# Kernel optimization log

Measured on AMD Instinct MI355X. Metric: run time of the kernel, lower is better.

## Reference

```python
import jax, jax.numpy as jnp
import numpy as np

D = 1024
H = 8          # MHA fallback num_heads
DH = D // H
DFF = 4096     # mlp_ratio * hidden_size
EPS = 1e-6


def _ln(x, g, b):
    mu = jnp.mean(x, axis=-1, keepdims=True)
    var = jnp.mean((x - mu) ** 2, axis=-1, keepdims=True)
    return (x - mu) * jax.lax.rsqrt(var + EPS) * g + b


def setup_inputs() -> dict:
    key = jax.random.key(0)
    ks = jax.random.split(key, 16)
    s = 0.02
    return {
        "x": jax.random.normal(ks[0], (8, 1024, D), jnp.float32),
        "c": jax.random.normal(ks[1], (8, D), jnp.float32),
        # Mamba-block (attention fallback) params
        "m_ada_w": jax.random.normal(ks[2], (D, 3 * D), jnp.float32) * s,
        "m_ada_b": jnp.zeros((3 * D,), jnp.float32),
        "m_norm_g": jnp.ones((D,), jnp.float32),
        "m_norm_b": jnp.zeros((D,), jnp.float32),
        "in_proj_w": jax.random.normal(ks[3], (3 * D, D), jnp.float32) * s,
        "in_proj_b": jnp.zeros((3 * D,), jnp.float32),
        "out_proj_w": jax.random.normal(ks[4], (D, D), jnp.float32) * s,
        "out_proj_b": jnp.zeros((D,), jnp.float32),
        # FeedForward-block params
        "f_ada_w": jax.random.normal(ks[5], (D, 3 * D), jnp.float32) * s,
        "f_ada_b": jnp.zeros((3 * D,), jnp.float32),
        "f_norm_g": jnp.ones((D,), jnp.float32),
        "f_norm_b": jnp.zeros((D,), jnp.float32),
        "w1": jax.random.normal(ks[6], (D, DFF), jnp.float32) * s,
        "b1": jnp.zeros((DFF,), jnp.float32),
        "w2": jax.random.normal(ks[7], (DFF, D), jnp.float32) * s,
        "b2": jnp.zeros((D,), jnp.float32),
    }


def reference(x, c, m_ada_w, m_ada_b, m_norm_g, m_norm_b, in_proj_w, in_proj_b,
              out_proj_w, out_proj_b, f_ada_w, f_ada_b, f_norm_g, f_norm_b,
              w1, b1, w2, b2):
    B, N, _ = x.shape
    # ---- MambaBlock (MHA fallback), dropout = identity (eval) ----
    mod = jax.nn.silu(c) @ m_ada_w + m_ada_b              # (B, 3D)
    shift, scale, gate = jnp.split(mod, 3, axis=-1)
    h = _ln(x, m_norm_g, m_norm_b)
    h = h * (1.0 + scale[:, None, :]) + shift[:, None, :]
    qkv = h @ in_proj_w.T + in_proj_b                      # (B, N, 3D)
    q, k, v = jnp.split(qkv, 3, axis=-1)
    q = q.reshape(B, N, H, DH)
    k = k.reshape(B, N, H, DH)
    v = v.reshape(B, N, H, DH)
    scores = jnp.einsum("bqhd,bkhd->bhqk", q, k) / np.sqrt(DH).astype(np.float32)
    attn = jax.nn.softmax(scores, axis=-1)
    o = jnp.einsum("bhqk,bkhd->bqhd", attn, v).reshape(B, N, D)
    o = o @ out_proj_w.T + out_proj_b
    x = x + gate[:, None, :] * o
    # ---- FeedForward block ----
    mod2 = jax.nn.silu(c) @ f_ada_w + f_ada_b
    shift2, scale2, gate2 = jnp.split(mod2, 3, axis=-1)
    h = _ln(x, f_norm_g, f_norm_b)
    h = h * (1.0 + scale2[:, None, :]) + shift2[:, None, :]
    h = jax.nn.gelu(h @ w1 + b1, approximate=False) @ w2 + b2
    return x + gate2[:, None, :] * h
```

## Files before the change

### kernel.cpp

```cpp
#include <hip/hip_runtime.h>

typedef __bf16 bf16x8 __attribute__((ext_vector_type(8)));
typedef float f32x4 __attribute__((ext_vector_type(4)));

__device__ __forceinline__ unsigned short f2bf(float f) {
    unsigned int u = __float_as_uint(f);
    unsigned int r = (u + 0x7FFFu + ((u >> 16) & 1u)) >> 16;
    return (unsigned short)r;
}

__device__ __forceinline__ void gload16(const void* g, void* l) {
    __builtin_amdgcn_global_load_lds(
        (const __attribute__((address_space(1))) unsigned int*)g,
        (__attribute__((address_space(3))) unsigned int*)l, 16, 0, 0);
}

__device__ __forceinline__ void barrier_raw() {
    asm volatile("" ::: "memory");
    __builtin_amdgcn_s_barrier();
    asm volatile("" ::: "memory");
}

__device__ __forceinline__ void vmwait0() {
    asm volatile("s_waitcnt vmcnt(0)" ::: "memory");
}

__device__ __forceinline__ float gelu_fast(float u) {
    float z = 1.595769122f * u + 0.071354816f * u * u * u;
    return u / (1.f + __expf(-z));
}

__global__ __launch_bounds__(256) void f2b4(const float* __restrict__ in,
                                            unsigned short* __restrict__ out) {
    size_t i = ((size_t)blockIdx.x * 256 + threadIdx.x) * 4;
    float4 v = *(const float4*)(in + i);
    ushort4 o;
    o.x = f2bf(v.x); o.y = f2bf(v.y); o.z = f2bf(v.z); o.w = f2bf(v.w);
    *(ushort4*)(out + i) = o;
}

__global__ __launch_bounds__(256) void transpose_f2b(const float* __restrict__ in,
                                                     unsigned short* __restrict__ out,
                                                     int R, int C) {
    __shared__ float tile[32][33];
    int r0 = blockIdx.y * 32, c0 = blockIdx.x * 32;
    int tx = threadIdx.x & 31, ty = threadIdx.x >> 5;
#pragma unroll
    for (int i = 0; i < 4; i++) {
        int r = ty + i * 8;
        tile[r][tx] = in[(size_t)(r0 + r) * C + c0 + tx];
    }
    __syncthreads();
#pragma unroll
    for (int i = 0; i < 4; i++) {
        int r = ty + i * 8;
        out[(size_t)(c0 + r) * R + r0 + tx] = f2bf(tile[tx][r]);
    }
}

__global__ __launch_bounds__(256) void ada_mod_part(const float* __restrict__ c,
                                                    const float* __restrict__ W,
                                                    float* __restrict__ partial) {
    __shared__ float sc[8 * 64];
    int kc = blockIdx.y * 64;
    for (int i = threadIdx.x; i < 512; i += 256) {
        int b = i >> 6, k = i & 63;
        float cv = c[b * 1024 + kc + k];
        sc[i] = cv / (1.f + __expf(-cv));
    }
    __syncthreads();
    int j = blockIdx.x * 256 + threadIdx.x;
    float acc[8] = {0, 0, 0, 0, 0, 0, 0, 0};
    for (int k = 0; k < 64; k++) {
        float w = W[(size_t)(kc + k) * 3072 + j];
#pragma unroll
        for (int b = 0; b < 8; b++) acc[b] += sc[b * 64 + k] * w;
    }
#pragma unroll
    for (int b = 0; b < 8; b++) partial[((size_t)blockIdx.y * 8 + b) * 3072 + j] = acc[b];
}

__global__ __launch_bounds__(256) void ada_reduce(const float* __restrict__ partial,
                                                  const float* __restrict__ bias,
                                                  float* __restrict__ out) {
    int idx = blockIdx.x * 256 + threadIdx.x;
    int b = idx / 3072;
    int jj = idx - b * 3072;
    float s = bias[jj];
#pragma unroll
    for (int ch = 0; ch < 16; ch++) s += partial[((size_t)ch * 8 + b) * 3072 + jj];
    out[idx] = s;
}

__global__ __launch_bounds__(256) void ln_mod_kernel(const float* __restrict__ x,
                                                     const float* __restrict__ gamma,
                                                     const float* __restrict__ beta,
                                                     const float* __restrict__ mods,
                                                     unsigned short* __restrict__ out) {
    int row = blockIdx.x;
    int b = row >> 10;
    float4 v = ((const float4*)(x + (size_t)row * 1024))[threadIdx.x];
    float s = v.x + v.y + v.z + v.w;
    float s2 = v.x * v.x + v.y * v.y + v.z * v.z + v.w * v.w;
#pragma unroll
    for (int d = 1; d < 64; d <<= 1) { s += __shfl_xor(s, d); s2 += __shfl_xor(s2, d); }
    __shared__ float red[8];
    int lane = threadIdx.x & 63, wid = threadIdx.x >> 6;
    if (lane == 0) { red[wid] = s; red[4 + wid] = s2; }
    __syncthreads();
    float S = red[0] + red[1] + red[2] + red[3];
    float S2 = red[4] + red[5] + red[6] + red[7];
    float mu = S * (1.f / 1024.f);
    float var = S2 * (1.f / 1024.f) - mu * mu;
    float rs = rsqrtf(var + 1e-6f);
    const float* mrow = mods + b * 3072;
    int j0 = threadIdx.x * 4;
    float hv[4] = {v.x, v.y, v.z, v.w};
    ushort4 o;
    unsigned short* op = (unsigned short*)&o;
#pragma unroll
    for (int i = 0; i < 4; i++) {
        int j = j0 + i;
        float hh = (hv[i] - mu) * rs * gamma[j] + beta[j];
        hh = hh * (1.f + mrow[1024 + j]) + mrow[j];
        op[i] = f2bf(hh);
    }
    *(ushort4*)(out + (size_t)row * 1024 + j0) = o;
}

template <int EP>
__global__ __launch_bounds__(256, 2) void gemmw(const unsigned short* __restrict__ A,
                                                const unsigned short* __restrict__ Bt,
                                                int N, int K, int nx,
                                                const float* __restrict__ bias,
                                                unsigned short* __restrict__ outb,
                                                unsigned short* __restrict__ vt) {
    constexpr int AE = 128 * 32;
    constexpr int BE = 256 * 32;
    extern __shared__ __align__(16) char smem[];
    __bf16* As = (__bf16*)smem;
    __bf16* Bs = As + 3 * AE;

    int tid = threadIdx.x, lane = tid & 63, wid = tid >> 6;
    int t = lane & 15, g = lane >> 4;
    int xk2 = ((t >> 1) & 3) * 8;

    int nwg = gridDim.x, chunk = nwg >> 3;
    int swz = (blockIdx.x & 7) * chunk + (blockIdx.x >> 3);
    int bx = swz % nx, by = swz / nx;
    int rowA0 = by * 128, colB0 = bx * 256;

    int rin = tid >> 2, cblk = tid & 3;
    int scol = (cblk ^ ((rin >> 1) & 3)) * 8;

    auto stage = [&](int nb, int kt) {
        int k0 = kt << 5;
        gload16(A + (size_t)(rowA0 + rin) * K + k0 + scol, As + nb * AE + tid * 8);
        gload16(A + (size_t)(rowA0 + 64 + rin) * K + k0 + scol,
                As + nb * AE + 2048 + tid * 8);
#pragma unroll
        for (int sl = 0; sl < 4; sl++)
            gload16(Bt + (size_t)(colB0 + sl * 64 + rin) * K + k0 + scol,
                    Bs + nb * BE + sl * 2048 + tid * 8);
    };

    f32x4 acc[8][4];
#pragma unroll
    for (int m = 0; m < 8; m++)
#pragma unroll
        for (int n = 0; n < 4; n++) acc[m][n] = (f32x4){0.f, 0.f, 0.f, 0.f};

    int NT = K >> 5;
    stage(0, 0);
    if (NT > 1) {
        stage(1, 1);
        asm volatile("s_waitcnt vmcnt(6)" ::: "memory");
    } else {
        vmwait0();
    }
    barrier_raw();

    int cur = 0, tgt = 2;
#pragma unroll 1
    for (int kt = 0; kt < NT; ++kt) {
        bool deep = (kt + 2) < NT;
        bool more = (kt + 1) < NT;
        if (deep) stage(tgt, kt + 2);
        const __bf16* Ac = As + cur * AE;
        const __bf16* Bc = Bs + cur * BE;

        bf16x8 b[4];
#pragma unroll
        for (int n = 0; n < 4; n++)
            b[n] = *(const bf16x8*)&Bc[(wid * 64 + n * 16 + t) * 32 + ((g * 8) ^ xk2)];

        __builtin_amdgcn_s_setprio(1);
#pragma unroll
        for (int mh = 0; mh < 2; mh++) {
            bf16x8 a[4];
#pragma unroll
            for (int m4 = 0; m4 < 4; m4++)
                a[m4] = *(const bf16x8*)&Ac[(mh * 64 + m4 * 16 + t) * 32 + ((g * 8) ^ xk2)];
#pragma unroll
            for (int m4 = 0; m4 < 4; m4++)
#pragma unroll
                for (int n = 0; n < 4; n++)
                    acc[mh * 4 + m4][n] =
                        __builtin_amdgcn_mfma_f32_16x16x32_bf16(a[m4], b[n], acc[mh * 4 + m4][n], 0, 0, 0);
        }
        __builtin_amdgcn_s_setprio(0);

        if (more) {
            if (deep) {
                asm volatile("s_waitcnt vmcnt(6)" ::: "memory");
            } else {
                vmwait0();
            }
            barrier_raw();
        }
        cur = (cur == 2) ? 0 : cur + 1;
        tgt = (tgt == 2) ? 0 : tgt + 1;
    }

    int col0 = colB0 + wid * 64;
    bool vpart = (EP == 0) && (colB0 >= 2048);
#pragma unroll
    for (int m = 0; m < 8; m++)
#pragma unroll
        for (int n = 0; n < 4; n++) {
            int col = col0 + n * 16 + t;
            if (EP == 0 && vpart) {
                int hcol = col - 2048;
                int hh = hcol >> 7, d = hcol & 127;
                int bb = rowA0 >> 10;
                int ntok = (rowA0 + m * 16 + g * 4) & 1023;
                float bs = bias[col];
                ushort4 vv;
                vv.x = f2bf(acc[m][n][0] + bs);
                vv.y = f2bf(acc[m][n][1] + bs);
                vv.z = f2bf(acc[m][n][2] + bs);
                vv.w = f2bf(acc[m][n][3] + bs);
                *(ushort4*)(vt + (((size_t)(bb * 8 + hh) * 128 + d) * 1024 + ntok)) = vv;
            } else {
#pragma unroll
                for (int r = 0; r < 4; r++) {
                    int row = rowA0 + m * 16 + g * 4 + r;
                    float v = acc[m][n][r];
                    if (EP == 0) {
                        outb[(size_t)row * N + col] = f2bf(v + bias[col]);
                    } else {
                        outb[(size_t)row * N + col] = f2bf(gelu_fast(v + bias[col]));
                    }
                }
            }
        }
}

template <int EP>
__global__ __launch_bounds__(256, 4) void gemmo(const unsigned short* __restrict__ A,
                                                const unsigned short* __restrict__ Bt,
                                                int N, int K, int nx,
                                                const float* __restrict__ bias,
                                                const float* __restrict__ xres,
                                                const float* __restrict__ mods,
                                                float* __restrict__ outf) {
    constexpr int AE = 128 * 32;
    constexpr int BE = 128 * 32;
    extern __shared__ __align__(16) char smem[];
    __bf16* As = (__bf16*)smem;
    __bf16* Bs = As + 3 * AE;

    int tid = threadIdx.x, lane = tid & 63, wid = tid >> 6;
    int wr = wid >> 1, wc = wid & 1;
    int t = lane & 15, g = lane >> 4;
    int xk2 = ((t >> 1) & 3) * 8;

    int nwg = gridDim.x, chunk = nwg >> 3;
    int swz = (blockIdx.x & 7) * chunk + (blockIdx.x >> 3);
    int bx = swz % nx, by = swz / nx;
    int rowA0 = by * 128, colB0 = bx * 128;

    int rin = tid >> 2, cblk = tid & 3;
    int scol = (cblk ^ ((rin >> 1) & 3)) * 8;

    auto stage = [&](int nb, int kt) {
        int k0 = kt << 5;
        gload16(A + (size_t)(rowA0 + rin) * K + k0 + scol, As + nb * AE + tid * 8);
        gload16(A + (size_t)(rowA0 + 64 + rin) * K + k0 + scol,
                As + nb * AE + 2048 + tid * 8);
        gload16(Bt + (size_t)(colB0 + rin) * K + k0 + scol, Bs + nb * BE + tid * 8);
        gload16(Bt + (size_t)(colB0 + 64 + rin) * K + k0 + scol,
                Bs + nb * BE + 2048 + tid * 8);
    };

    f32x4 acc[4][4];
#pragma unroll
    for (int m = 0; m < 4; m++)
#pragma unroll
        for (int n = 0; n < 4; n++) acc[m][n] = (f32x4){0.f, 0.f, 0.f, 0.f};

    int NT = K >> 5;
    stage(0, 0);
    if (NT > 1) {
        stage(1, 1);
        asm volatile("s_waitcnt vmcnt(4)" ::: "memory");
    } else {
        vmwait0();
    }
    barrier_raw();

    int cur = 0, tgt = 2;
#pragma unroll 1
    for (int kt = 0; kt < NT; ++kt) {
        bool deep = (kt + 2) < NT;
        bool more = (kt + 1) < NT;
        if (deep) stage(tgt, kt + 2);
        const __bf16* Ac = As + cur * AE;
        const __bf16* Bc = Bs + cur * BE;

        bf16x8 a[4], b[4];
#pragma unroll
        for (int m = 0; m < 4; m++)
            a[m] = *(const bf16x8*)&Ac[(wr * 64 + m * 16 + t) * 32 + ((g * 8) ^ xk2)];
#pragma unroll
        for (int n = 0; n < 4; n++)
            b[n] = *(const bf16x8*)&Bc[(wc * 64 + n * 16 + t) * 32 + ((g * 8) ^ xk2)];

        __builtin_amdgcn_s_setprio(1);
#pragma unroll
        for (int m = 0; m < 4; m++)
#pragma unroll
            for (int n = 0; n < 4; n++)
                acc[m][n] = __builtin_amdgcn_mfma_f32_16x16x32_bf16(a[m], b[n], acc[m][n], 0, 0, 0);
        __builtin_amdgcn_s_setprio(0);

        if (more) {
            if (deep) {
                asm volatile("s_waitcnt vmcnt(4)" ::: "memory");
            } else {
                vmwait0();
            }
            barrier_raw();
        }
        cur = (cur == 2) ? 0 : cur + 1;
        tgt = (tgt == 2) ? 0 : tgt + 1;
    }

    int row0 = rowA0 + wr * 64, col0 = colB0 + wc * 64;
#pragma unroll
    for (int m = 0; m < 4; m++)
#pragma unroll
        for (int n = 0; n < 4; n++) {
            int col = col0 + n * 16 + t;
#pragma unroll
            for (int r = 0; r < 4; r++) {
                int row = row0 + m * 16 + g * 4 + r;
                float v = acc[m][n][r];
                int bb = row >> 10;
                float gt = mods[bb * 3072 + 2048 + col];
                if (EP == 1) {
                    outf[(size_t)row * 1024 + col] =
                        xres[(size_t)row * 1024 + col] + gt * (v + bias[col]);
                } else {
                    outf[(size_t)row * 1024 + col] += gt * (v + bias[col]);
                }
            }
        }
}

__global__ __launch_bounds__(512, 4) void attn_kernel(const unsigned short* __restrict__ qkv,
                                                      const unsigned short* __restrict__ vt,
                                                      unsigned short* __restrict__ o) {
    extern __shared__ __align__(16) char asmem[];
    __bf16* Ks = (__bf16*)asmem;
    __bf16* Vts = Ks + 2 * 64 * 128;

    int bid = blockIdx.x;
    int logical = (bid & 7) * 64 + (bid >> 3);
    int q0 = (logical & 7) * 128;
    int bh = logical >> 3;
    int b = bh >> 3, h = bh & 7;
    int tid = threadIdx.x, lane = tid & 63, w = tid >> 6;
    int t = lane & 15, g = lane >> 4;
    int swzt = (t & 7) << 4;

    const unsigned short* qbase = qkv + (size_t)(b * 1024) * 3072 + h * 128;
    int qrow = q0 + w * 16 + t;
    bf16x8 qf[4];
#pragma unroll
    for (int ks = 0; ks < 4; ks++)
        qf[ks] = *(const bf16x8*)(qbase + (size_t)qrow * 3072 + ks * 32 + g * 8);

    f32x4 Oa[8];
#pragma unroll
    for (int n = 0; n < 8; n++) Oa[n] = (f32x4){0.f, 0.f, 0.f, 0.f};
    float m_r = -1e30f, l_r = 0.f;
    const float scale = 0.08838834764831845f;

    int krow = tid >> 4;
    int ksrc = (((tid & 15) * 16) ^ ((krow & 7) << 4)) >> 1;
    int vrow = tid >> 3;
    int vsrc = (((tid & 7) * 16) ^ ((vrow & 7) << 4)) >> 1;
    const unsigned short* vtg = vt + (size_t)bh * 128 * 1024;

    auto stage = [&](int buf, int kv0) {
        const unsigned short* kb = qkv + (size_t)(b * 1024 + kv0) * 3072 + 1024 + h * 128;
#pragma unroll
        for (int cc = 0; cc < 2; cc++) {
            gload16(kb + (size_t)(cc * 32 + krow) * 3072 + ksrc,
                    (void*)(Ks + buf * 8192 + cc * 4096 + tid * 8));
            gload16(vtg + (size_t)(cc * 64 + vrow) * 1024 + kv0 + vsrc,
                    (void*)(Vts + buf * 8192 + cc * 4096 + tid * 8));
        }
    };

    stage(0, 0);
    vmwait0();
    barrier_raw();

#pragma unroll 1
    for (int tile = 0; tile < 16; ++tile) {
        int cur = tile & 1;
        bool more = tile < 15;
        if (more) stage(cur ^ 1, (tile + 1) * 64);
        const __bf16* Kc = Ks + cur * 8192;
        const __bf16* Vc = Vts + cur * 8192;

        f32x4 St[4];
#pragma unroll
        for (int n = 0; n < 4; n++) St[n] = (f32x4){0.f, 0.f, 0.f, 0.f};
        __builtin_amdgcn_s_setprio(1);
#pragma unroll
        for (int ks = 0; ks < 4; ks++) {
#pragma unroll
            for (int n = 0; n < 4; n++) {
                bf16x8 kf = *(const bf16x8*)&Kc[(n * 16 + t) * 128 + (((ks * 64 + g * 16) ^ swzt) >> 1)];
                St[n] = __builtin_amdgcn_mfma_f32_16x16x32_bf16(kf, qf[ks], St[n], 0, 0, 0);
            }
        }
        __builtin_amdgcn_s_setprio(0);

        float mx = -1e30f;
#pragma unroll
        for (int n = 0; n < 4; n++)
#pragma unroll
            for (int r = 0; r < 4; r++) mx = fmaxf(mx, St[n][r]);
        mx *= scale;
        mx = fmaxf(mx, __shfl_xor(mx, 16));
        mx = fmaxf(mx, __shfl_xor(mx, 32));
        float mn = fmaxf(m_r, mx);
        float alpha = __expf(m_r - mn);
        m_r = mn;
        float p[4][4];
        float rs = 0.f;
#pragma unroll
        for (int n = 0; n < 4; n++)
#pragma unroll
            for (int r = 0; r < 4; r++) {
                float pv = __expf(St[n][r] * scale - mn);
                p[n][r] = pv;
                rs += pv;
            }
        rs += __shfl_xor(rs, 16);
        rs += __shfl_xor(rs, 32);
        l_r = l_r * alpha + rs;

        unsigned P01[4], P23[4];
#pragma unroll
        for (int n = 0; n < 4; n++) {
            P01[n] = (unsigned)f2bf(p[n][0]) | ((unsigned)f2bf(p[n][1]) << 16);
            P23[n] = (unsigned)f2bf(p[n][2]) | ((unsigned)f2bf(p[n][3]) << 16);
        }

#pragma unroll
        for (int r = 0; r < 4; r++) {
            float ar = __shfl(alpha, (lane & 48) + g * 4 + r);
#pragma unroll
            for (int n2 = 0; n2 < 8; n2++) Oa[n2][r] *= ar;
        }

#pragma unroll
        for (int ks2 = 0; ks2 < 2; ks2++) {
            int e = ks2 * 2, od = ks2 * 2 + 1;
            unsigned s16a = (g < 2) ? P01[e] : P01[od];
            unsigned s16b = (g < 2) ? P23[e] : P23[od];
            unsigned s32a = (g & 1) ? P01[e] : P01[od];
            unsigned s32b = (g & 1) ? P23[e] : P23[od];
            unsigned s48a = (g >= 2) ? P01[e] : P01[od];
            unsigned s48b = (g >= 2) ? P23[e] : P23[od];
            unsigned r16a = __shfl_xor(s16a, 16), r16b = __shfl_xor(s16b, 16);
            unsigned r32a = __shfl_xor(s32a, 32), r32b = __shfl_xor(s32b, 32);
            unsigned r48a = __shfl_xor(s48a, 48), r48b = __shfl_xor(s48b, 48);
            union { unsigned u[4]; bf16x8 v; } pa;
            pa.u[0] = (g == 0) ? P01[e] : (g == 1) ? r48a : (g == 2) ? r32a : r16a;
            pa.u[1] = (g == 0) ? P23[e] : (g == 1) ? r48b : (g == 2) ? r32b : r16b;
            pa.u[2] = (g == 0) ? r16a : (g == 1) ? r32a : (g == 2) ? r48a : P01[od];
            pa.u[3] = (g == 0) ? r16b : (g == 1) ? r32b : (g == 2) ? r48b : P23[od];
            __builtin_amdgcn_s_setprio(1);
#pragma unroll
            for (int n2 = 0; n2 < 8; n2++) {
                bf16x8 vf = *(const bf16x8*)&Vc[(n2 * 16 + t) * 64 + (((ks2 * 64 + g * 16) ^ swzt) >> 1)];
                Oa[n2] = __builtin_amdgcn_mfma_f32_16x16x32_bf16(pa.v, vf, Oa[n2], 0, 0, 0);
            }
            __builtin_amdgcn_s_setprio(0);
        }

        if (more) {
            vmwait0();
            barrier_raw();
        }
    }

#pragma unroll
    for (int r = 0; r < 4; r++) {
        float lq = __shfl(l_r, (lane & 48) + g * 4 + r);
        float inv = 1.f / lq;
        int orow = q0 + w * 16 + g * 4 + r;
#pragma unroll
        for (int n2 = 0; n2 < 8; n2++)
            o[(size_t)(b * 1024 + orow) * 1024 + h * 128 + n2 * 16 + t] = f2bf(Oa[n2][r] * inv);
    }
}

extern "C" void kernel_launch(void* const* d_in, const int* in_sizes, int n_in,
                              void* d_out, int out_size, void* d_ws, size_t ws_size,
                              hipStream_t stream) {
    const float* x          = (const float*)d_in[0];
    const float* c          = (const float*)d_in[1];
    const float* m_ada_w    = (const float*)d_in[2];
    const float* m_ada_b    = (const float*)d_in[3];
    const float* m_norm_g   = (const float*)d_in[4];
    const float* m_norm_b   = (const float*)d_in[5];
    const float* in_proj_w  = (const float*)d_in[6];
    const float* in_proj_b  = (const float*)d_in[7];
    const float* out_proj_w = (const float*)d_in[8];
    const float* out_proj_b = (const float*)d_in[9];
    const float* f_ada_w    = (const float*)d_in[10];
    const float* f_ada_b    = (const float*)d_in[11];
    const float* f_norm_g   = (const float*)d_in[12];
    const float* f_norm_b   = (const float*)d_in[13];
    const float* w1         = (const float*)d_in[14];
    const float* b1         = (const float*)d_in[15];
    const float* w2         = (const float*)d_in[16];
    const float* b2         = (const float*)d_in[17];
    float* out = (float*)d_out;
    char* ws = (char*)d_ws;

    unsigned short* Wq   = (unsigned short*)(ws + 0);
    unsigned short* Wo   = (unsigned short*)(ws + 6291456);
    unsigned short* vt   = (unsigned short*)(ws + 8388608);
    unsigned short* W1t  = (unsigned short*)(ws + 8388608);
    unsigned short* W2t  = (unsigned short*)(ws + 16777216);
    float*          modm = (float*)(ws + 25165824);
    float*          modf = (float*)(ws + 25264128);
    unsigned short* hbuf = (unsigned short*)(ws + 25362432);
    float*          part = (float*)(ws + 25362432);
    float*          part2= (float*)(ws + 25362432 + 2097152);
    unsigned short* qkv  = (unsigned short*)(ws + 42139648);
    unsigned short* obuf = (unsigned short*)(ws + 92471296);
    unsigned short* h2   = (unsigned short*)(ws + 42139648);

    hipFuncSetAttribute((const void*)&gemmw<0>, hipFuncAttributeMaxDynamicSharedMemorySize, 73728);
    hipFuncSetAttribute((const void*)&gemmw<2>, hipFuncAttributeMaxDynamicSharedMemorySize, 73728);
    hipFuncSetAttribute((const void*)&gemmo<1>, hipFuncAttributeMaxDynamicSharedMemorySize, 49152);
    hipFuncSetAttribute((const void*)&gemmo<3>, hipFuncAttributeMaxDynamicSharedMemorySize, 49152);
    hipFuncSetAttribute((const void*)&attn_kernel, hipFuncAttributeMaxDynamicSharedMemorySize, 65536);

    hipLaunchKernelGGL(ada_mod_part, dim3(12, 16), dim3(256), 0, stream, c, m_ada_w, part);
    hipLaunchKernelGGL(ada_mod_part, dim3(12, 16), dim3(256), 0, stream, c, f_ada_w, part2);
    hipLaunchKernelGGL(ada_reduce, dim3(96), dim3(256), 0, stream, part, m_ada_b, modm);
    hipLaunchKernelGGL(ada_reduce, dim3(96), dim3(256), 0, stream, part2, f_ada_b, modf);

    hipLaunchKernelGGL(f2b4, dim3(3072), dim3(256), 0, stream, in_proj_w, Wq);
    hipLaunchKernelGGL(f2b4, dim3(1024), dim3(256), 0, stream, out_proj_w, Wo);

    hipLaunchKernelGGL(ln_mod_kernel, dim3(8192), dim3(256), 0, stream, x, m_norm_g, m_norm_b, modm, hbuf);
    hipLaunchKernelGGL(HIP_KERNEL_NAME(gemmw<0>), dim3(768), dim3(256), 73728, stream,
                       hbuf, Wq, 3072, 1024, 12, in_proj_b, qkv, vt);
    hipLaunchKernelGGL(attn_kernel, dim3(512), dim3(512), 65536, stream, qkv, vt, obuf);
    hipLaunchKernelGGL(HIP_KERNEL_NAME(gemmo<1>), dim3(512), dim3(256), 49152, stream,
                       obuf, Wo, 1024, 1024, 8, out_proj_b, x, modm, out);

    hipLaunchKernelGGL(transpose_f2b, dim3(128, 32), dim3(256), 0, stream, w1, W1t, 1024, 4096);
    hipLaunchKernelGGL(transpose_f2b, dim3(32, 128), dim3(256), 0, stream, w2, W2t, 4096, 1024);

    hipLaunchKernelGGL(ln_mod_kernel, dim3(8192), dim3(256), 0, stream, out, f_norm_g, f_norm_b, modf, hbuf);
    hipLaunchKernelGGL(HIP_KERNEL_NAME(gemmw<2>), dim3(1024), dim3(256), 73728, stream,
                       hbuf, W1t, 4096, 1024, 16, b1, h2, (unsigned short*)nullptr);
    hipLaunchKernelGGL(HIP_KERNEL_NAME(gemmo<3>), dim3(512), dim3(256), 49152, stream,
                       h2, W2t, 1024, 4096, 8, b2, (const float*)nullptr, modf, out);
}
```

Baseline: 386.6 us.

## Use 256x256 eight-wave GEMM tiles, lazy softmax rescale, merge ada launches

The wide GEMM moves from 128x256 tiles with 4 waves and triple buffering to 256x256 tiles with 8 waves and double buffering. Next-tile loads are issued in two halves between the MFMA groups. This raises data reuse per tile and cuts A/B traffic, at the cost of a shallower pipeline and a full vmcnt(0) wait every iteration. Attention now skips the running-max rescale unless some lane's max grows by more than 8, and the two ada modulation passes are merged into single launches using a grid z/y dimension.

```diff
diff --git a/kernel.cpp b/kernel.cpp
--- a/kernel.cpp
+++ b/kernel.cpp
@@ -59,8 +59,12 @@
 }
 
 __global__ __launch_bounds__(256) void ada_mod_part(const float* __restrict__ c,
-                                                    const float* __restrict__ W,
-                                                    float* __restrict__ partial) {
+                                                    const float* __restrict__ W0,
+                                                    const float* __restrict__ W1,
+                                                    float* __restrict__ p0,
+                                                    float* __restrict__ p1) {
+    const float* W = blockIdx.z ? W1 : W0;
+    float* partial = blockIdx.z ? p1 : p0;
     __shared__ float sc[8 * 64];
     int kc = blockIdx.y * 64;
     for (int i = threadIdx.x; i < 512; i += 256) {
@@ -80,9 +84,15 @@
     for (int b = 0; b < 8; b++) partial[((size_t)blockIdx.y * 8 + b) * 3072 + j] = acc[b];
 }
 
-__global__ __launch_bounds__(256) void ada_reduce(const float* __restrict__ partial,
-                                                  const float* __restrict__ bias,
-                                                  float* __restrict__ out) {
+__global__ __launch_bounds__(256) void ada_reduce(const float* __restrict__ p0,
+                                                  const float* __restrict__ p1,
+                                                  const float* __restrict__ b0,
+                                                  const float* __restrict__ b1,
+                                                  float* __restrict__ o0,
+                                                  float* __restrict__ o1) {
+    const float* partial = blockIdx.y ? p1 : p0;
+    const float* bias = blockIdx.y ? b1 : b0;
+    float* out = blockIdx.y ? o1 : o0;
     int idx = blockIdx.x * 256 + threadIdx.x;
     int b = idx / 3072;
     int jj = idx - b * 3072;
@@ -129,40 +139,44 @@
 }
 
 template <int EP>
-__global__ __launch_bounds__(256, 2) void gemmw(const unsigned short* __restrict__ A,
+__global__ __launch_bounds__(512, 2) void gemm9(const unsigned short* __restrict__ A,
                                                 const unsigned short* __restrict__ Bt,
                                                 int N, int K, int nx,
                                                 const float* __restrict__ bias,
                                                 unsigned short* __restrict__ outb,
                                                 unsigned short* __restrict__ vt) {
-    constexpr int AE = 128 * 32;
-    constexpr int BE = 256 * 32;
+    constexpr int TE = 256 * 32;
     extern __shared__ __align__(16) char smem[];
     __bf16* As = (__bf16*)smem;
-    __bf16* Bs = As + 3 * AE;
+    __bf16* Bs = As + 2 * TE;
 
     int tid = threadIdx.x, lane = tid & 63, wid = tid >> 6;
+    int wr = wid >> 2, wc = wid & 3;
     int t = lane & 15, g = lane >> 4;
     int xk2 = ((t >> 1) & 3) * 8;
 
     int nwg = gridDim.x, chunk = nwg >> 3;
     int swz = (blockIdx.x & 7) * chunk + (blockIdx.x >> 3);
     int bx = swz % nx, by = swz / nx;
-    int rowA0 = by * 128, colB0 = bx * 256;
+    int rowA0 = by * 256, colB0 = bx * 256;
 
     int rin = tid >> 2, cblk = tid & 3;
     int scol = (cblk ^ ((rin >> 1) & 3)) * 8;
 
-    auto stage = [&](int nb, int kt) {
+    auto stageA = [&](int nb, int kt) {
         int k0 = kt << 5;
-        gload16(A + (size_t)(rowA0 + rin) * K + k0 + scol, As + nb * AE + tid * 8);
-        gload16(A + (size_t)(rowA0 + 64 + rin) * K + k0 + scol,
-                As + nb * AE + 2048 + tid * 8);
-#pragma unroll
-        for (int sl = 0; sl < 4; sl++)
-            gload16(Bt + (size_t)(colB0 + sl * 64 + rin) * K + k0 + scol,
-                    Bs + nb * BE + sl * 2048 + tid * 8);
+        gload16(A + (size_t)(rowA0 + rin) * K + k0 + scol,
+                As + nb * TE + rin * 32 + cblk * 8);
+        gload16(A + (size_t)(rowA0 + 128 + rin) * K + k0 + scol,
+                As + nb * TE + 4096 + rin * 32 + cblk * 8);
     };
+    auto stageB = [&](int nb, int kt) {
+        int k0 = kt << 5;
+        gload16(Bt + (size_t)(colB0 + rin) * K + k0 + scol,
+                Bs + nb * TE + rin * 32 + cblk * 8);
+        gload16(Bt + (size_t)(colB0 + 128 + rin) * K + k0 + scol,
+                Bs + nb * TE + 4096 + rin * 32 + cblk * 8);
+    };
 
     f32x4 acc[8][4];
 #pragma unroll
@@ -171,58 +185,53 @@
         for (int n = 0; n < 4; n++) acc[m][n] = (f32x4){0.f, 0.f, 0.f, 0.f};
 
     int NT = K >> 5;
-    stage(0, 0);
-    if (NT > 1) {
-        stage(1, 1);
-        asm volatile("s_waitcnt vmcnt(6)" ::: "memory");
-    } else {
-        vmwait0();
-    }
+    stageA(0, 0); stageB(0, 0);
+    vmwait0();
     barrier_raw();
 
-    int cur = 0, tgt = 2;
 #pragma unroll 1
     for (int kt = 0; kt < NT; ++kt) {
-        bool deep = (kt + 2) < NT;
+        int cur = kt & 1, nb = cur ^ 1;
+        const __bf16* Ac = As + cur * TE;
+        const __bf16* Bc = Bs + cur * TE;
         bool more = (kt + 1) < NT;
-        if (deep) stage(tgt, kt + 2);
-        const __bf16* Ac = As + cur * AE;
-        const __bf16* Bc = Bs + cur * BE;
-
-        bf16x8 b[4];
+
+        bf16x8 b[4], a0[4];
 #pragma unroll
         for (int n = 0; n < 4; n++)
-            b[n] = *(const bf16x8*)&Bc[(wid * 64 + n * 16 + t) * 32 + ((g * 8) ^ xk2)];
-
+            b[n] = *(const bf16x8*)&Bc[(wc * 64 + n * 16 + t) * 32 + ((g * 8) ^ xk2)];
+#pragma unroll
+        for (int m = 0; m < 4; m++)
+            a0[m] = *(const bf16x8*)&Ac[(wr * 128 + m * 16 + t) * 32 + ((g * 8) ^ xk2)];
+        if (more) stageA(nb, kt + 1);
         __builtin_amdgcn_s_setprio(1);
 #pragma unroll
-        for (int mh = 0; mh < 2; mh++) {
-            bf16x8 a[4];
-#pragma unroll
-            for (int m4 = 0; m4 < 4; m4++)
-                a[m4] = *(const bf16x8*)&Ac[(mh * 64 + m4 * 16 + t) * 32 + ((g * 8) ^ xk2)];
-#pragma unroll
-            for (int m4 = 0; m4 < 4; m4++)
-#pragma unroll
-                for (int n = 0; n < 4; n++)
-                    acc[mh * 4 + m4][n] =
-                        __builtin_amdgcn_mfma_f32_16x16x32_bf16(a[m4], b[n], acc[mh * 4 + m4][n], 0, 0, 0);
-        }
+        for (int m = 0; m < 4; m++)
+#pragma unroll
+            for (int n = 0; n < 4; n++)
+                acc[m][n] = __builtin_amdgcn_mfma_f32_16x16x32_bf16(a0[m], b[n], acc[m][n], 0, 0, 0);
         __builtin_amdgcn_s_setprio(0);
 
+        bf16x8 a1[4];
+#pragma unroll
+        for (int m = 0; m < 4; m++)
+            a1[m] = *(const bf16x8*)&Ac[(wr * 128 + 64 + m * 16 + t) * 32 + ((g * 8) ^ xk2)];
+        if (more) stageB(nb, kt + 1);
+        __builtin_amdgcn_s_setprio(1);
+#pragma unroll
+        for (int m = 0; m < 4; m++)
+#pragma unroll
+            for (int n = 0; n < 4; n++)
+                acc[4 + m][n] = __builtin_amdgcn_mfma_f32_16x16x32_bf16(a1[m], b[n], acc[4 + m][n], 0, 0, 0);
+        __builtin_amdgcn_s_setprio(0);
+
         if (more) {
-            if (deep) {
-                asm volatile("s_waitcnt vmcnt(6)" ::: "memory");
-            } else {
-                vmwait0();
-            }
+            vmwait0();
             barrier_raw();
         }
-        cur = (cur == 2) ? 0 : cur + 1;
-        tgt = (tgt == 2) ? 0 : tgt + 1;
-    }
-
-    int col0 = colB0 + wid * 64;
+    }
+
+    int col0 = colB0 + wc * 64;
     bool vpart = (EP == 0) && (colB0 >= 2048);
 #pragma unroll
     for (int m = 0; m < 8; m++)
@@ -231,20 +240,21 @@
             int col = col0 + n * 16 + t;
             if (EP == 0 && vpart) {
                 int hcol = col - 2048;
-                int hh = hcol >> 7, d = hcol & 127;
-                int bb = rowA0 >> 10;
-                int ntok = (rowA0 + m * 16 + g * 4) & 1023;
+                int hh = hcol >> 7, dd = hcol & 127;
+                int row0 = rowA0 + wr * 128 + m * 16 + g * 4;
+                int bb = row0 >> 10;
+                int ntok = row0 & 1023;
                 float bs = bias[col];
                 ushort4 vv;
                 vv.x = f2bf(acc[m][n][0] + bs);
                 vv.y = f2bf(acc[m][n][1] + bs);
                 vv.z = f2bf(acc[m][n][2] + bs);
                 vv.w = f2bf(acc[m][n][3] + bs);
-                *(ushort4*)(vt + (((size_t)(bb * 8 + hh) * 128 + d) * 1024 + ntok)) = vv;
+                *(ushort4*)(vt + (((size_t)(bb * 8 + hh) * 128 + dd) * 1024 + ntok)) = vv;
             } else {
 #pragma unroll
                 for (int r = 0; r < 4; r++) {
-                    int row = rowA0 + m * 16 + g * 4 + r;
+                    int row = rowA0 + wr * 128 + m * 16 + g * 4 + r;
                     float v = acc[m][n][r];
                     if (EP == 0) {
                         outb[(size_t)row * N + col] = f2bf(v + bias[col]);
@@ -448,35 +458,37 @@
         mx *= scale;
         mx = fmaxf(mx, __shfl_xor(mx, 16));
         mx = fmaxf(mx, __shfl_xor(mx, 32));
-        float mn = fmaxf(m_r, mx);
-        float alpha = __expf(m_r - mn);
-        m_r = mn;
+        if (!__all(mx - m_r <= 8.f)) {
+            float mn = fmaxf(m_r, mx);
+            float alpha = __expf(m_r - mn);
+            m_r = mn;
+            l_r *= alpha;
+#pragma unroll
+            for (int r = 0; r < 4; r++) {
+                float ar = __shfl(alpha, (lane & 48) + g * 4 + r);
+#pragma unroll
+                for (int n2 = 0; n2 < 8; n2++) Oa[n2][r] *= ar;
+            }
+        }
         float p[4][4];
         float rs = 0.f;
 #pragma unroll
         for (int n = 0; n < 4; n++)
 #pragma unroll
             for (int r = 0; r < 4; r++) {
-                float pv = __expf(St[n][r] * scale - mn);
+                float pv = __expf(St[n][r] * scale - m_r);
                 p[n][r] = pv;
                 rs += pv;
             }
         rs += __shfl_xor(rs, 16);
         rs += __shfl_xor(rs, 32);
-        l_r = l_r * alpha + rs;
+        l_r += rs;
 
         unsigned P01[4], P23[4];
 #pragma unroll
         for (int n = 0; n < 4; n++) {
             P01[n] = (unsigned)f2bf(p[n][0]) | ((unsigned)f2bf(p[n][1]) << 16);
             P23[n] = (unsigned)f2bf(p[n][2]) | ((unsigned)f2bf(p[n][3]) << 16);
-        }
-
-#pragma unroll
-        for (int r = 0; r < 4; r++) {
-            float ar = __shfl(alpha, (lane & 48) + g * 4 + r);
-#pragma unroll
-            for (int n2 = 0; n2 < 8; n2++) Oa[n2][r] *= ar;
         }
 
 #pragma unroll
@@ -560,22 +572,22 @@
     unsigned short* obuf = (unsigned short*)(ws + 92471296);
     unsigned short* h2   = (unsigned short*)(ws + 42139648);
 
-    hipFuncSetAttribute((const void*)&gemmw<0>, hipFuncAttributeMaxDynamicSharedMemorySize, 73728);
-    hipFuncSetAttribute((const void*)&gemmw<2>, hipFuncAttributeMaxDynamicSharedMemorySize, 73728);
+    hipFuncSetAttribute((const void*)&gemm9<0>, hipFuncAttributeMaxDynamicSharedMemorySize, 65536);
+    hipFuncSetAttribute((const void*)&gemm9<2>, hipFuncAttributeMaxDynamicSharedMemorySize, 65536);
     hipFuncSetAttribute((const void*)&gemmo<1>, hipFuncAttributeMaxDynamicSharedMemorySize, 49152);
     hipFuncSetAttribute((const void*)&gemmo<3>, hipFuncAttributeMaxDynamicSharedMemorySize, 49152);
     hipFuncSetAttribute((const void*)&attn_kernel, hipFuncAttributeMaxDynamicSharedMemorySize, 65536);
 
-    hipLaunchKernelGGL(ada_mod_part, dim3(12, 16), dim3(256), 0, stream, c, m_ada_w, part);
-    hipLaunchKernelGGL(ada_mod_part, dim3(12, 16), dim3(256), 0, stream, c, f_ada_w, part2);
-    hipLaunchKernelGGL(ada_reduce, dim3(96), dim3(256), 0, stream, part, m_ada_b, modm);
-    hipLaunchKernelGGL(ada_reduce, dim3(96), dim3(256), 0, stream, part2, f_ada_b, modf);
+    hipLaunchKernelGGL(ada_mod_part, dim3(12, 16, 2), dim3(256), 0, stream,
+                       c, m_ada_w, f_ada_w, part, part2);
+    hipLaunchKernelGGL(ada_reduce, dim3(96, 2), dim3(256), 0, stream,
+                       part, part2, m_ada_b, f_ada_b, modm, modf);
 
     hipLaunchKernelGGL(f2b4, dim3(3072), dim3(256), 0, stream, in_proj_w, Wq);
     hipLaunchKernelGGL(f2b4, dim3(1024), dim3(256), 0, stream, out_proj_w, Wo);
 
     hipLaunchKernelGGL(ln_mod_kernel, dim3(8192), dim3(256), 0, stream, x, m_norm_g, m_norm_b, modm, hbuf);
-    hipLaunchKernelGGL(HIP_KERNEL_NAME(gemmw<0>), dim3(768), dim3(256), 73728, stream,
+    hipLaunchKernelGGL(HIP_KERNEL_NAME(gemm9<0>), dim3(384), dim3(512), 65536, stream,
                        hbuf, Wq, 3072, 1024, 12, in_proj_b, qkv, vt);
     hipLaunchKernelGGL(attn_kernel, dim3(512), dim3(512), 65536, stream, qkv, vt, obuf);
     hipLaunchKernelGGL(HIP_KERNEL_NAME(gemmo<1>), dim3(512), dim3(256), 49152, stream,
@@ -585,7 +597,7 @@
     hipLaunchKernelGGL(transpose_f2b, dim3(32, 128), dim3(256), 0, stream, w2, W2t, 4096, 1024);
 
     hipLaunchKernelGGL(ln_mod_kernel, dim3(8192), dim3(256), 0, stream, out, f_norm_g, f_norm_b, modf, hbuf);
-    hipLaunchKernelGGL(HIP_KERNEL_NAME(gemmw<2>), dim3(1024), dim3(256), 73728, stream,
+    hipLaunchKernelGGL(HIP_KERNEL_NAME(gemm9<2>), dim3(512), dim3(512), 65536, stream,
                        hbuf, W1t, 4096, 1024, 16, b1, h2, (unsigned short*)nullptr);
     hipLaunchKernelGGL(HIP_KERNEL_NAME(gemmo<3>), dim3(512), dim3(256), 49152, stream,
                        h2, W2t, 1024, 4096, 8, b2, (const float*)nullptr, modf, out);
```

After: 377.8 us. 1.02x faster.
